# Optimization experiments

Measured on AMD Instinct MI355X. Metric: run time of the kernel, lower is better.

## Reference

```python
import jax, jax.numpy as jnp
import numpy as np

DEPTH, DIM, DIN, DM, NST, RNK, CSTEM, NCLS = 4, 64, 128, 256, 16, 8, 32, 16
EPS = 1e-5


def silu(x):
    return x * jax.nn.sigmoid(x)


def layernorm(x, g, b):
    m = x.mean(-1, keepdims=True)
    v = x.var(-1, keepdims=True)
    return (x - m) / jnp.sqrt(v + EPS) * g + b


def bn3d(x, g, b, m, v):  # eval-mode BatchNorm3d, x [B,C,T,H,W]
    s = g / jnp.sqrt(v + EPS)
    return x * s[None, :, None, None, None] + (b - m * s)[None, :, None, None, None]


def dwconv3d_same(x, w, b):  # x [B,C,T,H,W], w [C,1,3,3,3]
    y = jax.lax.conv_general_dilated(x, w, (1, 1, 1), 'SAME',
                                     feature_group_count=x.shape[1],
                                     dimension_numbers=('NCDHW', 'OIDHW', 'NCDHW'))
    return y + b[None, :, None, None, None]


def mamba(u, in_w, conv_w, conv_b, xproj_w, dtproj_w, dtproj_b, Alog, Dp, out_w):
    # u: [b, L, DIN]; mamba_ssm Mamba(d_model=DIN, d_state=16, expand=2, d_conv=4)
    b, L, _ = u.shape
    xz = u @ in_w.T                                  # [b,L,2*DM]
    x, z = jnp.split(xz, 2, axis=-1)                 # [b,L,DM] each
    # causal depthwise conv1d, kernel 4, left-pad 3
    xc = jnp.moveaxis(x, 1, 2)                       # [b,DM,L]
    xc = jnp.pad(xc, ((0, 0), (0, 0), (3, 0)))
    xc = jax.lax.conv_general_dilated(xc, conv_w, (1,), 'VALID',
                                      feature_group_count=conv_w.shape[0],
                                      dimension_numbers=('NCH', 'OIH', 'NCH'))
    xc = xc + conv_b[None, :, None]
    x = silu(jnp.moveaxis(xc, 2, 1))                 # [b,L,DM]
    dbc = x @ xproj_w.T                              # [b,L,RNK+2*NST]
    dt, Bc, Cc = jnp.split(dbc, [RNK, RNK + NST], axis=-1)
    dt = jax.nn.softplus(dt @ dtproj_w.T + dtproj_b)  # [b,L,DM]
    A = -jnp.exp(Alog)                               # [DM,NST]

    def step(h, inp):
        dt_l, u_l, B_l, C_l = inp                    # [b,DM],[b,DM],[b,NST],[b,NST]
        dA = jnp.exp(dt_l[..., None] * A)            # [b,DM,NST]
        h = dA * h + (dt_l * u_l)[..., None] * B_l[:, None, :]
        y = jnp.einsum('bdn,bn->bd', h, C_l)
        return h, y

    xs = (jnp.moveaxis(dt, 1, 0), jnp.moveaxis(x, 1, 0),
          jnp.moveaxis(Bc, 1, 0), jnp.moveaxis(Cc, 1, 0))
    h0 = jnp.zeros((b, DM, NST), x.dtype)
    _, ys = jax.lax.scan(step, h0, xs)               # ys [L,b,DM]
    y = jnp.moveaxis(ys, 0, 1) + x * Dp              # D skip
    y = y * silu(z)
    return y @ out_w.T                               # [b,L,DIN]


def setup_inputs() -> dict:
    key = jax.random.key(0)
    ks = iter(jax.random.split(key, 64))

    def rn(shape, s=0.02):
        return jax.random.normal(next(ks), shape, jnp.float32) * s

    D = DEPTH
    inp = {
        'x': jax.random.normal(next(ks), (32, 1, 32, 13, 13), jnp.float32),
        # R(2+1)D stem
        'sconv_w': rn((CSTEM, 1, 1, 3, 3), 0.1),
        'bn1_g': jnp.ones((CSTEM,)), 'bn1_b': jnp.zeros((CSTEM,)),
        'bn1_m': rn((CSTEM,), 0.1),
        'bn1_v': jax.random.uniform(next(ks), (CSTEM,), jnp.float32, 0.5, 1.5),
        'tconv_w': rn((CSTEM, 1, 3, 1, 1), 0.2),
        'bn2_g': jnp.ones((CSTEM,)), 'bn2_b': jnp.zeros((CSTEM,)),
        'bn2_m': rn((CSTEM,), 0.1),
        'bn2_v': jax.random.uniform(next(ks), (CSTEM,), jnp.float32, 0.5, 1.5),
        'last_w': rn((2 * CSTEM, CSTEM, 1, 1, 1), 0.1),
        # per-block params, stacked over depth
        'ln1_g': jnp.ones((D, DIM)), 'ln1_b': jnp.zeros((D, DIM)),
        'in_proj_w': rn((D, 2 * DIN, DIM)),
        'conv3d_w': rn((D, DIN, 1, 3, 3, 3), 0.1), 'conv3d_b': rn((D, DIN), 0.1),
        'm_in_w': rn((D, 2 * DM, DIN)),
        'm_conv_w': rn((D, DM, 1, 4), 0.2), 'm_conv_b': rn((D, DM), 0.1),
        'm_xproj_w': rn((D, RNK + 2 * NST, DM)),
        'm_dtproj_w': rn((D, DM, RNK), 0.1), 'm_dtproj_b': rn((D, DM), 0.1),
        'm_Alog': jnp.log(jax.random.uniform(next(ks), (D, DM, NST), jnp.float32, 1.0, 16.0)),
        'm_D': jnp.ones((D, DM)),
        'm_out_w': rn((D, DIN, DM)),
        'out_proj_w': rn((D, DIM, DIN)),
        'ln2_g': jnp.ones((D, DIM)), 'ln2_b': jnp.zeros((D, DIM)),
        'fc1_w': rn((D, 4 * DIM, DIM)), 'fc1_b': rn((D, 4 * DIM), 0.1),
        'fc2_w': rn((D, DIM, 4 * DIM)), 'fc2_b': rn((D, DIM), 0.1),
        'head_w': rn((NCLS, DIM)), 'head_b': jnp.zeros((NCLS,)),
    }
    return inp


def reference(x, sconv_w, bn1_g, bn1_b, bn1_m, bn1_v, tconv_w, bn2_g, bn2_b, bn2_m,
              bn2_v, last_w, ln1_g, ln1_b, in_proj_w, conv3d_w, conv3d_b, m_in_w,
              m_conv_w, m_conv_b, m_xproj_w, m_dtproj_w, m_dtproj_b, m_Alog, m_D,
              m_out_w, out_proj_w, ln2_g, ln2_b, fc1_w, fc1_b, fc2_w, fc2_b,
              head_w, head_b):
    dn = ('NCDHW', 'OIDHW', 'NCDHW')
    # R(2+1)D stem: spatial conv -> BN -> ReLU -> temporal dwconv -> BN -> ReLU -> 1x1x1
    h = jax.lax.conv_general_dilated(x, sconv_w, (1, 1, 1), 'VALID', dimension_numbers=dn)
    h = jax.nn.relu(bn3d(h, bn1_g, bn1_b, bn1_m, bn1_v))
    h = jax.lax.conv_general_dilated(h, tconv_w, (1, 1, 1), 'VALID',
                                     feature_group_count=CSTEM, dimension_numbers=dn)
    h = jax.nn.relu(bn3d(h, bn2_g, bn2_b, bn2_m, bn2_v))
    h = jax.lax.conv_general_dilated(h, last_w, (1, 1, 1), 'VALID', dimension_numbers=dn)
    xb = jnp.transpose(h, (0, 2, 3, 4, 1))  # [B, T', H', W', DIM]

    for i in range(DEPTH):
        # --- SSM branch ---
        hx = layernorm(xb, ln1_g[i], ln1_b[i])
        xz = hx @ in_proj_w[i].T                       # [B,T,H,W,2*DIN]
        xs_, z = jnp.split(xz, 2, axis=-1)
        z = silu(z)
        xc = jnp.moveaxis(xs_, 4, 1)                   # [B,DIN,T,H,W]
        xc = silu(dwconv3d_same(xc, conv3d_w[i], conv3d_b[i]))
        b, c, t, hh, ww = xc.shape
        seq = jnp.moveaxis(xc.reshape(b, c, t * hh * ww), 1, 2)  # [B,L,DIN]
        seq2 = jnp.concatenate([seq, seq[:, ::-1]], axis=0)      # [2B,L,DIN]
        y2 = mamba(seq2, m_in_w[i], m_conv_w[i], m_conv_b[i], m_xproj_w[i],
                   m_dtproj_w[i], m_dtproj_b[i], m_Alog[i], m_D[i], m_out_w[i])
        y = y2[:b] + y2[b:, ::-1]
        y = y.reshape(b, t, hh, ww, c) * z
        xb = xb + y @ out_proj_w[i].T
        # --- MLP branch ---
        h2 = layernorm(xb, ln2_g[i], ln2_b[i])
        h2 = jax.nn.gelu(h2 @ fc1_w[i].T + fc1_b[i], approximate=False)
        xb = xb + h2 @ fc2_w[i].T + fc2_b[i]

    feature = xb.mean(axis=(1, 2, 3))                  # [B, DIM]
    logits = feature @ head_w.T + head_b               # [B, NCLS]
    return (logits, feature)
```

## Files before the change

### kernel.cpp

```cpp
#include <hip/hip_runtime.h>
#include <hip/hip_bf16.h>
#include <hip/hip_fp16.h>

#define LL    3630
#define EPSV  1e-5f
#define NCH   33
#define CLEN  110

typedef short bf16x8 __attribute__((ext_vector_type(8)));
typedef float f32x4  __attribute__((ext_vector_type(4)));

__device__ __forceinline__ float bf2f(__hip_bfloat16 x){ return __bfloat162float(x); }
__device__ __forceinline__ __hip_bfloat16 f2bf(float x){ return __float2bfloat16(x); }
__device__ __forceinline__ float siluf(float x){ return x / (1.f + __expf(-x)); }

__global__ __launch_bounds__(256) void convert_weights(
    const float* __restrict__ s0, const float* __restrict__ s1,
    const float* __restrict__ s2, const float* __restrict__ s3,
    const float* __restrict__ s4, const float* __restrict__ s5,
    const float* __restrict__ s6,
    __hip_bfloat16* __restrict__ dst)
{
  int gid = blockIdx.x*256 + threadIdx.x;
  float v;
  if      (gid <  65536) v = s0[gid];
  else if (gid < 327680) v = s1[gid-65536];
  else if (gid < 458752) v = s2[gid-327680];
  else if (gid < 491520) v = s3[gid-458752];
  else if (gid < 557056) v = s4[gid-491520];
  else if (gid < 622592) v = s5[gid-557056];
  else if (gid < 671744){
    int rel = gid - 622592;
    int layer = rel / 12288;
    int rr  = (rel % 12288) / 256;
    int ccol= rel & 255;
    v = (rr < 40) ? s6[layer*10240 + rr*256 + ccol] : 0.f;
  }
  else return;
  dst[gid] = f2bf(v);
}

__global__ __launch_bounds__(256) void stem1_kernel(
    const float* __restrict__ x, const float* __restrict__ w,
    const float* __restrict__ g, const float* __restrict__ bb,
    const float* __restrict__ mm, const float* __restrict__ vv,
    float* __restrict__ out, int nb, int b0)
{
  int idx = blockIdx.x*256 + threadIdx.x;
  if (idx >= nb*123904) return;
  int j = idx % 11;
  int i = (idx/11) % 11;
  int t = (idx/121) % 32;
  int c = (idx/(121*32)) % 32;
  int b = idx/(121*32*32);
  const float* xp = x + ((b0+b)*32 + t)*169;
  const float* wp = w + c*9;
  float acc = 0.f;
  #pragma unroll
  for (int di=0; di<3; ++di)
    #pragma unroll
    for (int dj=0; dj<3; ++dj)
      acc += xp[(i+di)*13 + (j+dj)] * wp[di*3+dj];
  float s = g[c]*rsqrtf(vv[c]+EPSV);
  acc = acc*s + (bb[c]-mm[c]*s);
  out[idx] = fmaxf(acc, 0.f);
}

__global__ __launch_bounds__(256) void stem2_kernel(
    const float* __restrict__ h1, const float* __restrict__ w,
    const float* __restrict__ g, const float* __restrict__ bb,
    const float* __restrict__ mm, const float* __restrict__ vv,
    float* __restrict__ out, int nb)
{
  int idx = blockIdx.x*256 + threadIdx.x;
  if (idx >= nb*116160) return;
  int ij = idx % 121;
  int t  = (idx/121) % 30;
  int c  = (idx/(121*30)) % 32;
  int b  = idx/(121*30*32);
  const float* hp = h1 + ((b*32+c)*32)*121 + ij;
  const float* wp = w + c*3;
  float acc = 0.f;
  #pragma unroll
  for (int k=0;k<3;++k) acc += hp[(t+k)*121] * wp[k];
  float s = g[c]*rsqrtf(vv[c]+EPSV);
  acc = acc*s + (bb[c]-mm[c]*s);
  out[idx] = fmaxf(acc, 0.f);
}

__global__ __launch_bounds__(256) void stem3_kernel(
    const float* __restrict__ h2, const float* __restrict__ w,
    __hip_bfloat16* __restrict__ xb, int tokens)
{
  int gid = blockIdx.x*256 + threadIdx.x;
  int cc = gid & 63;
  int tok = gid >> 6;
  if (tok >= tokens) return;
  int ij = tok % 121;
  int t  = (tok/121) % 30;
  int b  = tok/LL;
  const float* hp = h2 + ((long)b*32)*30*121 + t*121 + ij;
  const float* wp = w + cc*32;
  float acc = 0.f;
  #pragma unroll
  for (int ci=0; ci<32; ++ci) acc += hp[ci*3630] * wp[ci];
  xb[(long)tok*64+cc] = f2bf(acc);
}

__global__ __launch_bounds__(256) void ln_kernel(
    const __hip_bfloat16* __restrict__ xb, const float* __restrict__ g,
    const float* __restrict__ b2, __hip_bfloat16* __restrict__ out, int tokens)
{
  int wid = threadIdx.x >> 6, lane = threadIdx.x & 63;
  long tok = (long)blockIdx.x*4 + wid;
  if (tok >= tokens) return;
  float v = bf2f(xb[tok*64 + lane]);
  float s = v, q = v*v;
  #pragma unroll
  for (int m=1; m<64; m<<=1){ s += __shfl_xor(s,m); q += __shfl_xor(q,m); }
  float mean = s*(1.f/64.f);
  float var  = q*(1.f/64.f) - mean*mean;
  float o = (v-mean)*rsqrtf(var+EPSV)*g[lane] + b2[lane];
  out[tok*64+lane] = f2bf(o);
}

template<int EPI>
__global__ __launch_bounds__(256) void gemm_bf16(
    const __hip_bfloat16* __restrict__ A, const __hip_bfloat16* __restrict__ W,
    int K, int N, int NH, int tokens,
    __hip_bfloat16* __restrict__ out1, __hip_bfloat16* __restrict__ out2,
    const float* __restrict__ bias, const __hip_bfloat16* __restrict__ gate,
    __hip_bfloat16* __restrict__ resid)
{
  int w   = threadIdx.x >> 6;
  int lane= threadIdx.x & 63;
  int r16 = lane & 15;
  int kg  = lane >> 4;
  long m0 = (long)blockIdx.x*128 + w*32;
  int  n0 = blockIdx.y*64;
  long ra0 = m0 + r16;      if (ra0 > tokens-1) ra0 = tokens-1;
  long ra1 = m0 + 16 + r16; if (ra1 > tokens-1) ra1 = tokens-1;
  f32x4 acc[2][4] = { { {0,0,0,0},{0,0,0,0},{0,0,0,0},{0,0,0,0} },
                      { {0,0,0,0},{0,0,0,0},{0,0,0,0},{0,0,0,0} } };
  for (int k0 = 0; k0 < K; k0 += 32){
    bf16x8 a0 = *reinterpret_cast<const bf16x8*>(A + ra0*K + k0 + kg*8);
    bf16x8 a1 = *reinterpret_cast<const bf16x8*>(A + ra1*K + k0 + kg*8);
    #pragma unroll
    for (int f=0; f<4; ++f){
      bf16x8 b = *reinterpret_cast<const bf16x8*>(W + (long)(n0 + f*16 + r16)*K + k0 + kg*8);
      acc[0][f] = __builtin_amdgcn_mfma_f32_16x16x32_bf16(a0, b, acc[0][f], 0, 0, 0);
      acc[1][f] = __builtin_amdgcn_mfma_f32_16x16x32_bf16(a1, b, acc[1][f], 0, 0, 0);
    }
  }
  #pragma unroll
  for (int g2=0; g2<2; ++g2){
    #pragma unroll
    for (int f=0; f<4; ++f){
      int col = n0 + f*16 + r16;
      #pragma unroll
      for (int r=0; r<4; ++r){
        long row = m0 + g2*16 + kg*4 + r;
        if (row >= tokens) continue;
        float v = acc[g2][f][r];
        if (EPI == 0){
          if (col < NH) out1[row*NH + col] = f2bf(v);
          else          out2[row*NH + col - NH] = f2bf(siluf(v));
        } else if (EPI == 2){
          v += bias[col];
          v = 0.5f*v*(1.f + erff(v*0.70710678118f));
          out1[row*N + col] = f2bf(v);
        } else if (EPI == 3){
          if (bias) v += bias[col];
          resid[row*N + col] = f2bf(v + bf2f(resid[row*N + col]));
        } else {
          out1[row*N + col] = f2bf(v * bf2f(gate[row*N + col]));
        }
      }
    }
  }
}

__global__ __launch_bounds__(256) void dwconv3d_kernel(
    const __hip_bfloat16* __restrict__ xs, const float* __restrict__ w,
    const float* __restrict__ bias, __hip_bfloat16* __restrict__ seq, int tokens)
{
  long gid = (long)blockIdx.x*256 + threadIdx.x;
  int c = gid & 127;
  long tok = gid >> 7;
  if (tok >= tokens) return;
  int j  = tok % 11;
  int i2 = (tok/11) % 11;
  int t  = (tok/121) % 30;
  long b = tok/LL;
  const float* wc = w + c*27;
  float acc = bias[c];
  #pragma unroll
  for (int dt=0; dt<3; ++dt){
    int tt = t+dt-1; if (tt<0 || tt>=30) continue;
    #pragma unroll
    for (int di=0; di<3; ++di){
      int ii = i2+di-1; if (ii<0 || ii>=11) continue;
      #pragma unroll
      for (int dj=0; dj<3; ++dj){
        int jj = j+dj-1; if (jj<0 || jj>=11) continue;
        long t2 = (b*30+tt)*121 + ii*11 + jj;
        acc += wc[dt*9+di*3+dj] * bf2f(xs[t2*128 + c]);
      }
    }
  }
  seq[tok*128 + c] = f2bf(siluf(acc));
}

__global__ __launch_bounds__(256) void mamba_pre_kernel(
    const __hip_bfloat16* __restrict__ xm,
    const float* __restrict__ cw, const float* __restrict__ cbv,
    const __hip_bfloat16* __restrict__ xpw_bf,
    __hip_bfloat16* __restrict__ ub,
    float* __restrict__ pre,
    int nb)
{
  __shared__ __hip_bfloat16 xcs[64][264];
  int s  = blockIdx.x / 57;
  int ch = blockIdx.x % 57;
  int p0 = ch*64;
  int b  = s % nb;
  bool fwd = s < nb;
  int d = threadIdx.x;
  const long basex = (long)b*LL*256 + d;
  const long sLL = (long)s*LL;
  float w0=cw[d*4], w1=cw[d*4+1], w2=cw[d*4+2], w3=cw[d*4+3], cb=cbv[d];
  float p1=0.f, p2=0.f, p3=0.f;
  if (p0-1 >= 0) p1 = bf2f(xm[basex + (long)(fwd ? p0-1 : LL-p0  )*256]);
  if (p0-2 >= 0) p2 = bf2f(xm[basex + (long)(fwd ? p0-2 : LL+1-p0)*256]);
  if (p0-3 >= 0) p3 = bf2f(xm[basex + (long)(fwd ? p0-3 : LL+2-p0)*256]);
  for (int t=0; t<64; ++t){
    int p = p0 + t;
    float xl = 0.f;
    if (p < LL) xl = bf2f(xm[basex + (long)(fwd ? p : LL-1-p)*256]);
    float xc = w3*xl + w2*p1 + w1*p2 + w0*p3 + cb;
    p3=p2; p2=p1; p1=xl;
    __hip_bfloat16 uv = f2bf(siluf(xc));
    xcs[t][d] = uv;
    if (p < LL) ub[(sLL + p)*256 + d] = uv;
  }
  __syncthreads();
  int w = threadIdx.x >> 6, lane = threadIdx.x & 63;
  int r16 = lane & 15, kg = lane >> 4;
  int t0 = w*16;
  f32x4 acc[3] = { {0,0,0,0},{0,0,0,0},{0,0,0,0} };
  for (int k0=0; k0<256; k0+=32){
    bf16x8 a = *reinterpret_cast<const bf16x8*>(&xcs[t0+r16][k0+kg*8]);
    #pragma unroll
    for (int f=0; f<3; ++f){
      bf16x8 bb = *reinterpret_cast<const bf16x8*>(xpw_bf + (f*16+r16)*256 + k0 + kg*8);
      acc[f] = __builtin_amdgcn_mfma_f32_16x16x32_bf16(a, bb, acc[f], 0, 0, 0);
    }
  }
  #pragma unroll
  for (int f=0; f<3; ++f){
    int col = f*16 + r16;
    #pragma unroll
    for (int r=0; r<4; ++r){
      int tl = t0 + kg*4 + r;
      int p = p0 + tl;
      if (p >= LL) continue;
      if (col < 40) pre[(sLL + p)*40 + col] = acc[f][r];
    }
  }
}

__global__ __launch_bounds__(256) void scan_p1(
    const __hip_bfloat16* __restrict__ ub,
    const float* __restrict__ pre,
    const float* __restrict__ dtw, const float* __restrict__ dtbv,
    const float* __restrict__ Alog,
    float* __restrict__ hfin, float* __restrict__ sdt)
{
  int d = threadIdx.x;
  int sc = blockIdx.x;
  int ch = sc % NCH, s = sc / NCH;
  float a2[16];
  #pragma unroll
  for (int n=0;n<16;++n) a2[n] = -__expf(Alog[d*16+n]) * 1.44269504f;
  float dw[8];
  #pragma unroll
  for (int r=0;r<8;++r) dw[r] = dtw[d*8+r];
  float dtb_d = dtbv[d];
  float h[16];
  #pragma unroll
  for (int n=0;n<16;++n) h[n] = 0.f;
  float sacc = 0.f;
  long tok0 = (long)s*LL + ch*CLEN;
  long ui = tok0*256 + d;
  long pi = tok0*40;
  for (int l=0; l<CLEN; ++l){
    float u = bf2f(ub[ui]);
    float4 r0 = *reinterpret_cast<const float4*>(pre+pi);
    float4 r1 = *reinterpret_cast<const float4*>(pre+pi+4);
    float xacc = dtb_d;
    xacc = fmaf(r0.x,dw[0],fmaf(r0.y,dw[1],fmaf(r0.z,dw[2],fmaf(r0.w,dw[3],xacc))));
    xacc = fmaf(r1.x,dw[4],fmaf(r1.y,dw[5],fmaf(r1.z,dw[6],fmaf(r1.w,dw[7],xacc))));
    float dt = (xacc > 20.f) ? xacc : __logf(1.f + __expf(xacc));
    sacc += dt;
    float dtu = dt*u;
    float4 B0 = *reinterpret_cast<const float4*>(pre+pi+8);
    float4 B1 = *reinterpret_cast<const float4*>(pre+pi+12);
    float4 B2 = *reinterpret_cast<const float4*>(pre+pi+16);
    float4 B3 = *reinterpret_cast<const float4*>(pre+pi+20);
    float Bv[16];
    Bv[0]=B0.x; Bv[1]=B0.y; Bv[2]=B0.z; Bv[3]=B0.w;
    Bv[4]=B1.x; Bv[5]=B1.y; Bv[6]=B1.z; Bv[7]=B1.w;
    Bv[8]=B2.x; Bv[9]=B2.y; Bv[10]=B2.z; Bv[11]=B2.w;
    Bv[12]=B3.x; Bv[13]=B3.y; Bv[14]=B3.z; Bv[15]=B3.w;
    #pragma unroll
    for (int n=0;n<16;++n){
      float e = exp2f(dt*a2[n]);
      h[n] = fmaf(e, h[n], dtu*Bv[n]);
    }
    ui += 256; pi += 40;
  }
  long hbase = ((long)sc*256 + d)*16;
  #pragma unroll
  for (int n=0;n<16;++n) hfin[hbase+n] = h[n];
  sdt[(long)sc*256 + d] = sacc;
}

__global__ __launch_bounds__(256) void scan_comb(
    const float* __restrict__ Alog,
    float* __restrict__ hfin, const float* __restrict__ sdt)
{
  int s = blockIdx.x >> 4, dg = blockIdx.x & 15;
  int d = dg*16 + (threadIdx.x >> 4), n = threadIdx.x & 15;
  float a2 = -__expf(Alog[d*16+n]) * 1.44269504f;
  float h = 0.f;
  for (int ch=0; ch<NCH; ++ch){
    long sc = (long)s*NCH + ch;
    long idx = (sc*256 + d)*16 + n;
    float hf = hfin[idx];
    float sd = sdt[sc*256 + d];
    hfin[idx] = h;
    h = exp2f(a2*sd)*h + hf;
  }
}

__global__ __launch_bounds__(256) void scan_p2(
    __hip_bfloat16* __restrict__ ub,
    const float* __restrict__ pre,
    const float* __restrict__ dtw, const float* __restrict__ dtbv,
    const float* __restrict__ Alog, const float* __restrict__ Dv,
    const float* __restrict__ hinit)
{
  int d = threadIdx.x;
  int sc = blockIdx.x;
  int ch = sc % NCH, s = sc / NCH;
  float a2[16];
  #pragma unroll
  for (int n=0;n<16;++n) a2[n] = -__expf(Alog[d*16+n]) * 1.44269504f;
  float dw[8];
  #pragma unroll
  for (int r=0;r<8;++r) dw[r] = dtw[d*8+r];
  float dtb_d = dtbv[d];
  float dpv = Dv[d];
  float h[16];
  long hbase = ((long)sc*256 + d)*16;
  #pragma unroll
  for (int n=0;n<16;++n) h[n] = hinit[hbase+n];
  int l0 = ch*CLEN;
  long tok0 = (long)s*LL + l0;
  long ui = tok0*256 + d;
  long pi = tok0*40;
  for (int l=0; l<CLEN; ++l){
    float u = bf2f(ub[ui]);
    float4 r0 = *reinterpret_cast<const float4*>(pre+pi);
    float4 r1 = *reinterpret_cast<const float4*>(pre+pi+4);
    float xacc = dtb_d;
    xacc = fmaf(r0.x,dw[0],fmaf(r0.y,dw[1],fmaf(r0.z,dw[2],fmaf(r0.w,dw[3],xacc))));
    xacc = fmaf(r1.x,dw[4],fmaf(r1.y,dw[5],fmaf(r1.z,dw[6],fmaf(r1.w,dw[7],xacc))));
    float dt = (xacc > 20.f) ? xacc : __logf(1.f + __expf(xacc));
    float dtu = dt*u;
    float4 B0 = *reinterpret_cast<const float4*>(pre+pi+8);
    float4 B1 = *reinterpret_cast<const float4*>(pre+pi+12);
    float4 B2 = *reinterpret_cast<const float4*>(pre+pi+16);
    float4 B3 = *reinterpret_cast<const float4*>(pre+pi+20);
    float4 C0 = *reinterpret_cast<const float4*>(pre+pi+24);
    float4 C1 = *reinterpret_cast<const float4*>(pre+pi+28);
    float4 C2 = *reinterpret_cast<const float4*>(pre+pi+32);
    float4 C3 = *reinterpret_cast<const float4*>(pre+pi+36);
    float Bv[16], Cv[16];
    Bv[0]=B0.x; Bv[1]=B0.y; Bv[2]=B0.z; Bv[3]=B0.w;
    Bv[4]=B1.x; Bv[5]=B1.y; Bv[6]=B1.z; Bv[7]=B1.w;
    Bv[8]=B2.x; Bv[9]=B2.y; Bv[10]=B2.z; Bv[11]=B2.w;
    Bv[12]=B3.x; Bv[13]=B3.y; Bv[14]=B3.z; Bv[15]=B3.w;
    Cv[0]=C0.x; Cv[1]=C0.y; Cv[2]=C0.z; Cv[3]=C0.w;
    Cv[4]=C1.x; Cv[5]=C1.y; Cv[6]=C1.z; Cv[7]=C1.w;
    Cv[8]=C2.x; Cv[9]=C2.y; Cv[10]=C2.z; Cv[11]=C2.w;
    Cv[12]=C3.x; Cv[13]=C3.y; Cv[14]=C3.z; Cv[15]=C3.w;
    float y = 0.f;
    #pragma unroll
    for (int n=0;n<16;++n){
      float e = exp2f(dt*a2[n]);
      h[n] = fmaf(e, h[n], dtu*Bv[n]);
      y = fmaf(h[n], Cv[n], y);
    }
    ub[ui] = f2bf(y + u*dpv);
    ui += 256; pi += 40;
  }
}

__global__ __launch_bounds__(256) void combine_kernel(
    const __hip_bfloat16* __restrict__ yb, const __hip_bfloat16* __restrict__ zm,
    __hip_bfloat16* __restrict__ ycomb, int tokens, int nb)
{
  long gid = (long)blockIdx.x*256 + threadIdx.x;
  long tok = gid >> 8;
  if (tok >= tokens) return;
  int c = gid & 255;
  long l = tok % LL, b = tok / LL;
  float vf = bf2f(yb[( b*LL + l)*256 + c]);
  float vb = bf2f(yb[((nb+b)*LL + (LL-1-l))*256 + c]);
  ycomb[gid] = f2bf((vf+vb)*bf2f(zm[gid]));
}

__global__ __launch_bounds__(256) void head1_kernel(
    const __hip_bfloat16* __restrict__ xb, float* __restrict__ hp)
{
  __shared__ float partial[4][64];
  int b = blockIdx.x / 30, ch = blockIdx.x % 30;
  int d = threadIdx.x & 63, part = threadIdx.x >> 6;
  float acc = 0.f;
  int lend = (ch+1)*121;
  for (int l = ch*121 + part; l < lend; l += 4)
    acc += bf2f(xb[((long)b*LL + l)*64 + d]);
  partial[part][d] = acc;
  __syncthreads();
  if (part == 0)
    hp[(b*30 + ch)*64 + d] = partial[0][d]+partial[1][d]+partial[2][d]+partial[3][d];
}

__global__ __launch_bounds__(64) void head2_kernel(
    const float* __restrict__ hp, const float* __restrict__ hw,
    const float* __restrict__ hb, float* __restrict__ out, int b0)
{
  __shared__ float feat[64];
  int b = blockIdx.x;
  int d = threadIdx.x;
  float acc = 0.f;
  #pragma unroll
  for (int ch=0; ch<30; ++ch) acc += hp[(b*30+ch)*64 + d];
  float f = acc * (1.f/3630.f);
  feat[d] = f;
  out[512 + (b0+b)*64 + d] = f;
  __syncthreads();
  if (d < 16){
    float a2 = hb[d];
    #pragma unroll
    for (int k=0; k<64; ++k) a2 += feat[k]*hw[d*64+k];
    out[(b0+b)*16 + d] = a2;
  }
}

extern "C" void kernel_launch(void* const* d_in, const int* in_sizes, int n_in,
                              void* d_out, int out_size, void* d_ws, size_t ws_size,
                              hipStream_t stream)
{
  const float* x        = (const float*)d_in[0];
  const float* sconv_w  = (const float*)d_in[1];
  const float* bn1_g    = (const float*)d_in[2];
  const float* bn1_b    = (const float*)d_in[3];
  const float* bn1_m    = (const float*)d_in[4];
  const float* bn1_v    = (const float*)d_in[5];
  const float* tconv_w  = (const float*)d_in[6];
  const float* bn2_g    = (const float*)d_in[7];
  const float* bn2_b    = (const float*)d_in[8];
  const float* bn2_m    = (const float*)d_in[9];
  const float* bn2_v    = (const float*)d_in[10];
  const float* last_w   = (const float*)d_in[11];
  const float* ln1_g    = (const float*)d_in[12];
  const float* ln1_b    = (const float*)d_in[13];
  const float* in_proj_w= (const float*)d_in[14];
  const float* conv3d_w = (const float*)d_in[15];
  const float* conv3d_b = (const float*)d_in[16];
  const float* m_in_w   = (const float*)d_in[17];
  const float* m_conv_w = (const float*)d_in[18];
  const float* m_conv_b = (const float*)d_in[19];
  const float* m_xproj_w= (const float*)d_in[20];
  const float* m_dtproj_w=(const float*)d_in[21];
  const float* m_dtproj_b=(const float*)d_in[22];
  const float* m_Alog   = (const float*)d_in[23];
  const float* m_D      = (const float*)d_in[24];
  const float* m_out_w  = (const float*)d_in[25];
  const float* out_proj_w=(const float*)d_in[26];
  const float* ln2_g    = (const float*)d_in[27];
  const float* ln2_b    = (const float*)d_in[28];
  const float* fc1_w    = (const float*)d_in[29];
  const float* fc1_b    = (const float*)d_in[30];
  const float* fc2_w    = (const float*)d_in[31];
  const float* fc2_b    = (const float*)d_in[32];
  const float* head_w   = (const float*)d_in[33];
  const float* head_b   = (const float*)d_in[34];

  const size_t WB = 1345536;
  int nb = 1;
  for (int cand = 32; cand >= 1; cand >>= 1){
    size_t TPc = (((size_t)cand*LL + 63)/64)*64;
    size_t S2c = (size_t)2*cand*LL;
    size_t need = WB + TPc*2048 + S2c*672;
    if (need <= ws_size){ nb = cand; break; }
  }
  const size_t TP  = (((size_t)nb*LL + 63)/64)*64;
  const int S2  = 2*nb;
  const size_t S2T = (size_t)S2*LL;
  const int tokens = nb*LL;

  char* ws = (char*)d_ws;
  __hip_bfloat16* wbf   = (__hip_bfloat16*)(ws);
  size_t o = WB;
  __hip_bfloat16* xb    = (__hip_bfloat16*)(ws + o); o += TP*128;
  __hip_bfloat16* hx    = (__hip_bfloat16*)(ws + o); o += TP*128;
  float*          hp    = (float*)hx;
  __hip_bfloat16* xs    = (__hip_bfloat16*)(ws + o); o += TP*256;
  __hip_bfloat16* seq   = (__hip_bfloat16*)(ws + o); o += TP*256;
  __hip_bfloat16* ycomb = xs;
  float*          hfin  = (float*)xs;
  __hip_bfloat16* zblk  = (__hip_bfloat16*)(ws + o); o += TP*256;
  __hip_bfloat16* xm    = (__hip_bfloat16*)(ws + o);
  __hip_bfloat16* yo    = xm;                        o += TP*512;
  __hip_bfloat16* zm    = (__hip_bfloat16*)(ws + o);
  __hip_bfloat16* h2m   = zm;                        o += TP*512;
  float*          pre   = (float*)(ws + o);          o += S2T*160;
  __hip_bfloat16* ybuf  = (__hip_bfloat16*)(ws + o);
  float*          h1s   = (float*)(ws + o);
  float*          h2s   = (float*)(ws + o + (size_t)nb*495616);
  float*          sdtb  = hfin + (size_t)S2*NCH*4096;

  convert_weights<<<2624, 256, 0, stream>>>(in_proj_w, m_in_w, m_out_w, out_proj_w,
                                            fc1_w, fc2_w, m_xproj_w, wbf);

  const int gM2 = (int)((TP + 127)/128);

  for (int b0 = 0; b0 < 32; b0 += nb){
    stem1_kernel<<<nb*484, 256, 0, stream>>>(x, sconv_w, bn1_g, bn1_b, bn1_m, bn1_v, h1s, nb, b0);
    stem2_kernel<<<(nb*116160+255)/256, 256, 0, stream>>>(h1s, tconv_w, bn2_g, bn2_b, bn2_m, bn2_v, h2s, nb);
    stem3_kernel<<<(tokens*64+255)/256, 256, 0, stream>>>(h2s, last_w, xb, tokens);

    for (int i = 0; i < 4; ++i){
      ln_kernel<<<(tokens+3)/4, 256, 0, stream>>>(xb, ln1_g + i*64, ln1_b + i*64, hx, tokens);
      gemm_bf16<0><<<dim3(gM2,4), 256, 0, stream>>>(hx, wbf + i*16384, 64, 256, 128, tokens,
                                                    xs, zblk, nullptr, nullptr, nullptr);
      dwconv3d_kernel<<<(tokens*128+255)/256, 256, 0, stream>>>(xs, conv3d_w + i*3456, conv3d_b + i*128, seq, tokens);
      gemm_bf16<0><<<dim3(gM2,8), 256, 0, stream>>>(seq, wbf + 65536 + i*65536, 128, 512, 256, tokens,
                                                    xm, zm, nullptr, nullptr, nullptr);
      mamba_pre_kernel<<<S2*57, 256, 0, stream>>>(xm, m_conv_w + i*1024, m_conv_b + i*256,
                                                  wbf + 622592 + i*12288, ybuf, pre, nb);
      scan_p1<<<S2*NCH, 256, 0, stream>>>(ybuf, pre, m_dtproj_w + i*2048, m_dtproj_b + i*256,
                                          m_Alog + i*4096, hfin, sdtb);
      scan_comb<<<S2*16, 256, 0, stream>>>(m_Alog + i*4096, hfin, sdtb);
      scan_p2<<<S2*NCH, 256, 0, stream>>>(ybuf, pre, m_dtproj_w + i*2048, m_dtproj_b + i*256,
                                          m_Alog + i*4096, m_D + i*256, hfin);
      combine_kernel<<<(tokens*256+255)/256, 256, 0, stream>>>(ybuf, zm, ycomb, tokens, nb);
      gemm_bf16<4><<<dim3(gM2,2), 256, 0, stream>>>(ycomb, wbf + 327680 + i*32768, 256, 128, 0, tokens,
                                                    yo, nullptr, nullptr, zblk, nullptr);
      gemm_bf16<3><<<dim3(gM2,1), 256, 0, stream>>>(yo, wbf + 458752 + i*8192, 128, 64, 0, tokens,
                                                    nullptr, nullptr, nullptr, nullptr, xb);
      ln_kernel<<<(tokens+3)/4, 256, 0, stream>>>(xb, ln2_g + i*64, ln2_b + i*64, hx, tokens);
      gemm_bf16<2><<<dim3(gM2,4), 256, 0, stream>>>(hx, wbf + 491520 + i*16384, 64, 256, 0, tokens,
                                                    h2m, nullptr, fc1_b + i*256, nullptr, nullptr);
      gemm_bf16<3><<<dim3(gM2,1), 256, 0, stream>>>(h2m, wbf + 557056 + i*16384, 256, 64, 0, tokens,
                                                    nullptr, nullptr, fc2_b + i*64, nullptr, xb);
    }
    head1_kernel<<<nb*30, 256, 0, stream>>>(xb, hp);
    head2_kernel<<<nb, 64, 0, stream>>>(hp, head_w, head_b, (float*)d_out, b0);
  }
}
```

Before: 7.064 ms.

## Fuse layernorm into residual GEMM epilogues, pack scan math, vectorize combine

Adds a GEMM epilogue that applies bias and residual add, then computes the next layernorm in-register with 16-lane shuffles, writing both the residual and the normalized activation. This removes two standalone layernorm launches per block and their extra pass over the token tensor. The selective-scan kernels now use float2 vectors so the compiler can emit packed FMA/mul, and combine_kernel processes eight bf16 values per thread with 16-byte loads. The last block's fused LN computes an unused normalization, which costs a little extra work.

```diff
diff --git a/kernel.cpp b/kernel.cpp
--- a/kernel.cpp
+++ b/kernel.cpp
@@ -9,10 +9,14 @@
 
 typedef short bf16x8 __attribute__((ext_vector_type(8)));
 typedef float f32x4  __attribute__((ext_vector_type(4)));
+typedef float f32x2  __attribute__((ext_vector_type(2)));
+typedef float f32x16 __attribute__((ext_vector_type(16)));
 
 __device__ __forceinline__ float bf2f(__hip_bfloat16 x){ return __bfloat162float(x); }
 __device__ __forceinline__ __hip_bfloat16 f2bf(float x){ return __float2bfloat16(x); }
 __device__ __forceinline__ float siluf(float x){ return x / (1.f + __expf(-x)); }
+__device__ __forceinline__ float s2f(short s){ __hip_bfloat16 t = __builtin_bit_cast(__hip_bfloat16, s); return __bfloat162float(t); }
+__device__ __forceinline__ short f2s(float x){ __hip_bfloat16 t = __float2bfloat16(x); return __builtin_bit_cast(short, t); }
 
 __global__ __launch_bounds__(256) void convert_weights(
     const float* __restrict__ s0, const float* __restrict__ s1,
@@ -130,7 +134,8 @@
     int K, int N, int NH, int tokens,
     __hip_bfloat16* __restrict__ out1, __hip_bfloat16* __restrict__ out2,
     const float* __restrict__ bias, const __hip_bfloat16* __restrict__ gate,
-    __hip_bfloat16* __restrict__ resid)
+    __hip_bfloat16* __restrict__ resid,
+    const float* __restrict__ lng, const float* __restrict__ lnb)
 {
   int w   = threadIdx.x >> 6;
   int lane= threadIdx.x & 63;
@@ -151,6 +156,42 @@
       acc[0][f] = __builtin_amdgcn_mfma_f32_16x16x32_bf16(a0, b, acc[0][f], 0, 0, 0);
       acc[1][f] = __builtin_amdgcn_mfma_f32_16x16x32_bf16(a1, b, acc[1][f], 0, 0, 0);
     }
+  }
+  if (EPI == 5){
+    float gv[4], bv[4], biasv[4];
+    #pragma unroll
+    for (int f=0; f<4; ++f){
+      gv[f] = lng[f*16+r16]; bv[f] = lnb[f*16+r16];
+      biasv[f] = bias ? bias[f*16+r16] : 0.f;
+    }
+    #pragma unroll
+    for (int g2=0; g2<2; ++g2){
+      #pragma unroll
+      for (int r=0; r<4; ++r){
+        long row = m0 + g2*16 + kg*4 + r;
+        bool ok = row < tokens;
+        long rowc = ok ? row : (tokens-1);
+        float v[4]; float s = 0.f, q = 0.f;
+        #pragma unroll
+        for (int f=0; f<4; ++f){
+          float t = acc[g2][f][r] + biasv[f] + bf2f(resid[rowc*64 + f*16+r16]);
+          v[f] = t; s += t; q += t*t;
+        }
+        #pragma unroll
+        for (int m=1; m<16; m<<=1){ s += __shfl_xor(s,m); q += __shfl_xor(q,m); }
+        float mean = s*(1.f/64.f);
+        float var  = q*(1.f/64.f) - mean*mean;
+        float rstd = rsqrtf(var+EPSV);
+        if (ok){
+          #pragma unroll
+          for (int f=0; f<4; ++f){
+            resid[row*64 + f*16+r16] = f2bf(v[f]);
+            out1 [row*64 + f*16+r16] = f2bf((v[f]-mean)*rstd*gv[f] + bv[f]);
+          }
+        }
+      }
+    }
+    return;
   }
   #pragma unroll
   for (int g2=0; g2<2; ++g2){
@@ -279,16 +320,17 @@
   int d = threadIdx.x;
   int sc = blockIdx.x;
   int ch = sc % NCH, s = sc / NCH;
-  float a2[16];
-  #pragma unroll
-  for (int n=0;n<16;++n) a2[n] = -__expf(Alog[d*16+n]) * 1.44269504f;
+  f32x2 a2[8], h[8];
+  #pragma unroll
+  for (int k=0;k<8;++k){
+    a2[k] = (f32x2){ -__expf(Alog[d*16+2*k])*1.44269504f,
+                     -__expf(Alog[d*16+2*k+1])*1.44269504f };
+    h[k] = (f32x2){0.f, 0.f};
+  }
   float dw[8];
   #pragma unroll
   for (int r=0;r<8;++r) dw[r] = dtw[d*8+r];
   float dtb_d = dtbv[d];
-  float h[16];
-  #pragma unroll
-  for (int n=0;n<16;++n) h[n] = 0.f;
   float sacc = 0.f;
   long tok0 = (long)s*LL + ch*CLEN;
   long ui = tok0*256 + d;
@@ -302,26 +344,22 @@
     xacc = fmaf(r1.x,dw[4],fmaf(r1.y,dw[5],fmaf(r1.z,dw[6],fmaf(r1.w,dw[7],xacc))));
     float dt = (xacc > 20.f) ? xacc : __logf(1.f + __expf(xacc));
     sacc += dt;
+    f32x16 B = *reinterpret_cast<const f32x16*>(pre+pi+8);
+    f32x2 dt2  = (f32x2){dt, dt};
     float dtu = dt*u;
-    float4 B0 = *reinterpret_cast<const float4*>(pre+pi+8);
-    float4 B1 = *reinterpret_cast<const float4*>(pre+pi+12);
-    float4 B2 = *reinterpret_cast<const float4*>(pre+pi+16);
-    float4 B3 = *reinterpret_cast<const float4*>(pre+pi+20);
-    float Bv[16];
-    Bv[0]=B0.x; Bv[1]=B0.y; Bv[2]=B0.z; Bv[3]=B0.w;
-    Bv[4]=B1.x; Bv[5]=B1.y; Bv[6]=B1.z; Bv[7]=B1.w;
-    Bv[8]=B2.x; Bv[9]=B2.y; Bv[10]=B2.z; Bv[11]=B2.w;
-    Bv[12]=B3.x; Bv[13]=B3.y; Bv[14]=B3.z; Bv[15]=B3.w;
-    #pragma unroll
-    for (int n=0;n<16;++n){
-      float e = exp2f(dt*a2[n]);
-      h[n] = fmaf(e, h[n], dtu*Bv[n]);
+    f32x2 dtu2 = (f32x2){dtu, dtu};
+    #pragma unroll
+    for (int k=0;k<8;++k){
+      f32x2 t = dt2*a2[k];
+      f32x2 e = (f32x2){ exp2f(t.x), exp2f(t.y) };
+      f32x2 bk = (f32x2){ B[2*k], B[2*k+1] };
+      h[k] = __builtin_elementwise_fma(e, h[k], dtu2*bk);
     }
     ui += 256; pi += 40;
   }
   long hbase = ((long)sc*256 + d)*16;
   #pragma unroll
-  for (int n=0;n<16;++n) hfin[hbase+n] = h[n];
+  for (int k=0;k<8;++k){ hfin[hbase+2*k] = h[k].x; hfin[hbase+2*k+1] = h[k].y; }
   sdt[(long)sc*256 + d] = sacc;
 }
 
@@ -353,18 +391,19 @@
   int d = threadIdx.x;
   int sc = blockIdx.x;
   int ch = sc % NCH, s = sc / NCH;
-  float a2[16];
-  #pragma unroll
-  for (int n=0;n<16;++n) a2[n] = -__expf(Alog[d*16+n]) * 1.44269504f;
+  f32x2 a2[8], h[8];
+  long hbase = ((long)sc*256 + d)*16;
+  #pragma unroll
+  for (int k=0;k<8;++k){
+    a2[k] = (f32x2){ -__expf(Alog[d*16+2*k])*1.44269504f,
+                     -__expf(Alog[d*16+2*k+1])*1.44269504f };
+    h[k] = (f32x2){ hinit[hbase+2*k], hinit[hbase+2*k+1] };
+  }
   float dw[8];
   #pragma unroll
   for (int r=0;r<8;++r) dw[r] = dtw[d*8+r];
   float dtb_d = dtbv[d];
   float dpv = Dv[d];
-  float h[16];
-  long hbase = ((long)sc*256 + d)*16;
-  #pragma unroll
-  for (int n=0;n<16;++n) h[n] = hinit[hbase+n];
   int l0 = ch*CLEN;
   long tok0 = (long)s*LL + l0;
   long ui = tok0*256 + d;
@@ -377,31 +416,22 @@
     xacc = fmaf(r0.x,dw[0],fmaf(r0.y,dw[1],fmaf(r0.z,dw[2],fmaf(r0.w,dw[3],xacc))));
     xacc = fmaf(r1.x,dw[4],fmaf(r1.y,dw[5],fmaf(r1.z,dw[6],fmaf(r1.w,dw[7],xacc))));
     float dt = (xacc > 20.f) ? xacc : __logf(1.f + __expf(xacc));
+    f32x16 B = *reinterpret_cast<const f32x16*>(pre+pi+8);
+    f32x16 C = *reinterpret_cast<const f32x16*>(pre+pi+24);
+    f32x2 dt2  = (f32x2){dt, dt};
     float dtu = dt*u;
-    float4 B0 = *reinterpret_cast<const float4*>(pre+pi+8);
-    float4 B1 = *reinterpret_cast<const float4*>(pre+pi+12);
-    float4 B2 = *reinterpret_cast<const float4*>(pre+pi+16);
-    float4 B3 = *reinterpret_cast<const float4*>(pre+pi+20);
-    float4 C0 = *reinterpret_cast<const float4*>(pre+pi+24);
-    float4 C1 = *reinterpret_cast<const float4*>(pre+pi+28);
-    float4 C2 = *reinterpret_cast<const float4*>(pre+pi+32);
-    float4 C3 = *reinterpret_cast<const float4*>(pre+pi+36);
-    float Bv[16], Cv[16];
-    Bv[0]=B0.x; Bv[1]=B0.y; Bv[2]=B0.z; Bv[3]=B0.w;
-    Bv[4]=B1.x; Bv[5]=B1.y; Bv[6]=B1.z; Bv[7]=B1.w;
-    Bv[8]=B2.x; Bv[9]=B2.y; Bv[10]=B2.z; Bv[11]=B2.w;
-    Bv[12]=B3.x; Bv[13]=B3.y; Bv[14]=B3.z; Bv[15]=B3.w;
-    Cv[0]=C0.x; Cv[1]=C0.y; Cv[2]=C0.z; Cv[3]=C0.w;
-    Cv[4]=C1.x; Cv[5]=C1.y; Cv[6]=C1.z; Cv[7]=C1.w;
-    Cv[8]=C2.x; Cv[9]=C2.y; Cv[10]=C2.z; Cv[11]=C2.w;
-    Cv[12]=C3.x; Cv[13]=C3.y; Cv[14]=C3.z; Cv[15]=C3.w;
-    float y = 0.f;
-    #pragma unroll
-    for (int n=0;n<16;++n){
-      float e = exp2f(dt*a2[n]);
-      h[n] = fmaf(e, h[n], dtu*Bv[n]);
-      y = fmaf(h[n], Cv[n], y);
-    }
+    f32x2 dtu2 = (f32x2){dtu, dtu};
+    f32x2 y2 = (f32x2){0.f, 0.f};
+    #pragma unroll
+    for (int k=0;k<8;++k){
+      f32x2 t = dt2*a2[k];
+      f32x2 e = (f32x2){ exp2f(t.x), exp2f(t.y) };
+      f32x2 bk = (f32x2){ B[2*k], B[2*k+1] };
+      f32x2 ck = (f32x2){ C[2*k], C[2*k+1] };
+      h[k] = __builtin_elementwise_fma(e, h[k], dtu2*bk);
+      y2 = __builtin_elementwise_fma(h[k], ck, y2);
+    }
+    float y = y2.x + y2.y;
     ub[ui] = f2bf(y + u*dpv);
     ui += 256; pi += 40;
   }
@@ -412,13 +442,20 @@
     __hip_bfloat16* __restrict__ ycomb, int tokens, int nb)
 {
   long gid = (long)blockIdx.x*256 + threadIdx.x;
-  long tok = gid >> 8;
+  long tok = gid >> 5;
   if (tok >= tokens) return;
-  int c = gid & 255;
+  int c8 = (gid & 31) * 8;
   long l = tok % LL, b = tok / LL;
-  float vf = bf2f(yb[( b*LL + l)*256 + c]);
-  float vb = bf2f(yb[((nb+b)*LL + (LL-1-l))*256 + c]);
-  ycomb[gid] = f2bf((vf+vb)*bf2f(zm[gid]));
+  bf16x8 vf = *reinterpret_cast<const bf16x8*>(yb + ( b*LL + l)*256 + c8);
+  bf16x8 vb = *reinterpret_cast<const bf16x8*>(yb + ((nb+b)*LL + (LL-1-l))*256 + c8);
+  bf16x8 zz = *reinterpret_cast<const bf16x8*>(zm + tok*256 + c8);
+  bf16x8 out;
+  #pragma unroll
+  for (int k=0;k<8;++k){
+    float r = (s2f(vf[k]) + s2f(vb[k])) * s2f(zz[k]);
+    out[k] = f2s(r);
+  }
+  *reinterpret_cast<bf16x8*>(ycomb + tok*256 + c8) = out;
 }
 
 __global__ __launch_bounds__(256) void head1_kernel(
@@ -542,14 +579,14 @@
     stem1_kernel<<<nb*484, 256, 0, stream>>>(x, sconv_w, bn1_g, bn1_b, bn1_m, bn1_v, h1s, nb, b0);
     stem2_kernel<<<(nb*116160+255)/256, 256, 0, stream>>>(h1s, tconv_w, bn2_g, bn2_b, bn2_m, bn2_v, h2s, nb);
     stem3_kernel<<<(tokens*64+255)/256, 256, 0, stream>>>(h2s, last_w, xb, tokens);
+    ln_kernel<<<(tokens+3)/4, 256, 0, stream>>>(xb, ln1_g, ln1_b, hx, tokens);
 
     for (int i = 0; i < 4; ++i){
-      ln_kernel<<<(tokens+3)/4, 256, 0, stream>>>(xb, ln1_g + i*64, ln1_b + i*64, hx, tokens);
       gemm_bf16<0><<<dim3(gM2,4), 256, 0, stream>>>(hx, wbf + i*16384, 64, 256, 128, tokens,
-                                                    xs, zblk, nullptr, nullptr, nullptr);
+                                                    xs, zblk, nullptr, nullptr, nullptr, nullptr, nullptr);
       dwconv3d_kernel<<<(tokens*128+255)/256, 256, 0, stream>>>(xs, conv3d_w + i*3456, conv3d_b + i*128, seq, tokens);
       gemm_bf16<0><<<dim3(gM2,8), 256, 0, stream>>>(seq, wbf + 65536 + i*65536, 128, 512, 256, tokens,
-                                                    xm, zm, nullptr, nullptr, nullptr);
+                                                    xm, zm, nullptr, nullptr, nullptr, nullptr, nullptr);
       mamba_pre_kernel<<<S2*57, 256, 0, stream>>>(xm, m_conv_w + i*1024, m_conv_b + i*256,
                                                   wbf + 622592 + i*12288, ybuf, pre, nb);
       scan_p1<<<S2*NCH, 256, 0, stream>>>(ybuf, pre, m_dtproj_w + i*2048, m_dtproj_b + i*256,
@@ -557,16 +594,18 @@
       scan_comb<<<S2*16, 256, 0, stream>>>(m_Alog + i*4096, hfin, sdtb);
       scan_p2<<<S2*NCH, 256, 0, stream>>>(ybuf, pre, m_dtproj_w + i*2048, m_dtproj_b + i*256,
                                           m_Alog + i*4096, m_D + i*256, hfin);
-      combine_kernel<<<(tokens*256+255)/256, 256, 0, stream>>>(ybuf, zm, ycomb, tokens, nb);
+      combine_kernel<<<(tokens*32+255)/256, 256, 0, stream>>>(ybuf, zm, ycomb, tokens, nb);
       gemm_bf16<4><<<dim3(gM2,2), 256, 0, stream>>>(ycomb, wbf + 327680 + i*32768, 256, 128, 0, tokens,
-                                                    yo, nullptr, nullptr, zblk, nullptr);
-      gemm_bf16<3><<<dim3(gM2,1), 256, 0, stream>>>(yo, wbf + 458752 + i*8192, 128, 64, 0, tokens,
-                                                    nullptr, nullptr, nullptr, nullptr, xb);
-      ln_kernel<<<(tokens+3)/4, 256, 0, stream>>>(xb, ln2_g + i*64, ln2_b + i*64, hx, tokens);
+                                                    yo, nullptr, nullptr, zblk, nullptr, nullptr, nullptr);
+      gemm_bf16<5><<<dim3(gM2,1), 256, 0, stream>>>(yo, wbf + 458752 + i*8192, 128, 64, 0, tokens,
+                                                    hx, nullptr, nullptr, nullptr, xb,
+                                                    ln2_g + i*64, ln2_b + i*64);
       gemm_bf16<2><<<dim3(gM2,4), 256, 0, stream>>>(hx, wbf + 491520 + i*16384, 64, 256, 0, tokens,
-                                                    h2m, nullptr, fc1_b + i*256, nullptr, nullptr);
-      gemm_bf16<3><<<dim3(gM2,1), 256, 0, stream>>>(h2m, wbf + 557056 + i*16384, 256, 64, 0, tokens,
-                                                    nullptr, nullptr, fc2_b + i*64, nullptr, xb);
+                                                    h2m, nullptr, fc1_b + i*256, nullptr, nullptr, nullptr, nullptr);
+      int inext = (i < 3) ? i+1 : 3;
+      gemm_bf16<5><<<dim3(gM2,1), 256, 0, stream>>>(h2m, wbf + 557056 + i*16384, 256, 64, 0, tokens,
+                                                    hx, nullptr, fc2_b + i*64, nullptr, xb,
+                                                    ln1_g + inext*64, ln1_b + inext*64);
     }
     head1_kernel<<<nb*30, 256, 0, stream>>>(xb, hp);
     head2_kernel<<<nb, 64, 0, stream>>>(hp, head_w, head_b, (float*)d_out, b0);
```

After: 6.706 ms. -5.1%, faster.
